# Kernel optimization log

Measured on AMD Instinct MI355X. Metric: run time of the kernel, lower is better.

Reference implementation:

```python
import jax, jax.numpy as jnp
import numpy as np

DIM_IN = 1024
DIM_K = 64
EPS = 1e-5

def setup_inputs() -> dict:
    key = jax.random.key(0)
    ks = jax.random.split(key, 9)
    s_in = 1.0 / np.sqrt(DIM_IN)
    s_k = 1.0 / np.sqrt(DIM_K)
    return {
        "X": jax.random.normal(ks[0], (8, 2048, DIM_IN), dtype=jnp.float32),
        "Wq": jax.random.uniform(ks[1], (DIM_IN, DIM_K), jnp.float32, -s_in, s_in),
        "bq": jax.random.uniform(ks[2], (DIM_K,), jnp.float32, -s_in, s_in),
        "Wk": jax.random.uniform(ks[3], (DIM_IN, DIM_K), jnp.float32, -s_in, s_in),
        "bk": jax.random.uniform(ks[4], (DIM_K,), jnp.float32, -s_in, s_in),
        "Wv": jax.random.uniform(ks[5], (DIM_IN, DIM_K), jnp.float32, -s_in, s_in),
        "bv": jax.random.uniform(ks[6], (DIM_K,), jnp.float32, -s_in, s_in),
        "Wo": jax.random.uniform(ks[7], (DIM_K, DIM_IN), jnp.float32, -s_k, s_k),
        "bo": jax.random.uniform(ks[8], (DIM_IN,), jnp.float32, -s_k, s_k),
        "gamma": jnp.ones((DIM_IN,), jnp.float32),
        "beta": jnp.zeros((DIM_IN,), jnp.float32),
    }

def reference(X, Wq, bq, Wk, bk, Wv, bv, Wo, bo, gamma, beta):
    q = X @ Wq + bq                       # [B,S,K]
    k = X @ Wk + bk
    v = X @ Wv + bv
    scores = jnp.einsum("bqk,bsk->bqs", q, k) / jnp.sqrt(jnp.float32(DIM_K))
    attn = jax.nn.softmax(scores, axis=2)  # [B,S,S]
    av = jnp.einsum("bqs,bsk->bqk", attn, v)
    y = X + av @ Wo + bo                  # residual, [B,S,D]
    mu = jnp.mean(y, axis=-1, keepdims=True)
    var = jnp.mean(jnp.square(y - mu), axis=-1, keepdims=True)
    return (y - mu) / jnp.sqrt(var + EPS) * gamma + beta
```

## Files before the change

### kernel.cpp

```cpp
#include <hip/hip_runtime.h>
#include <hip/hip_bf16.h>

#define DIM_D 1024
#define DIM_KH 64
#define SEQ   2048
#define BATCH 8
#define NROWS (BATCH*SEQ)
#define KVSPLIT 4
#define KEYS_PER_SPLIT (SEQ/KVSPLIT)

typedef __attribute__((ext_vector_type(8))) short short8;
typedef __attribute__((ext_vector_type(4))) short short4v;
typedef __attribute__((ext_vector_type(4))) float floatx4;

__device__ __forceinline__ ushort f2bf(float f) {
    union { __hip_bfloat16 h; ushort u; } cv;
    cv.h = __float2bfloat16(f);
    return cv.u;
}

__device__ __forceinline__ uint4 pack8(float4 a, float4 b) {
    uint4 p;
    p.x = (uint)f2bf(a.x) | ((uint)f2bf(a.y) << 16);
    p.y = (uint)f2bf(a.z) | ((uint)f2bf(a.w) << 16);
    p.z = (uint)f2bf(b.x) | ((uint)f2bf(b.y) << 16);
    p.w = (uint)f2bf(b.z) | ((uint)f2bf(b.w) << 16);
    return p;
}

__global__ void wcvt_kernel(const float* __restrict__ Wq,
                            const float* __restrict__ Wk,
                            const float* __restrict__ Wv,
                            ushort* __restrict__ WT)
{
    const int n  = blockIdx.x;
    const int o  = n >> 6;
    const int nn = n & 63;
    const float* W = (o == 0) ? Wq : (o == 1) ? Wk : Wv;
    #pragma unroll
    for (int i = 0; i < 4; i++) {
        int k = threadIdx.x + i * 256;
        WT[(size_t)n * DIM_D + k] = f2bf(W[(size_t)k * DIM_KH + nn]);
    }
}

__global__ void wocvt_kernel(const float* __restrict__ Wo, ushort* __restrict__ WoT)
{
    const int tid = threadIdx.x;
    const int n = blockIdx.x * 4 + (tid >> 6);
    const int k = tid & 63;
    WoT[(size_t)n * DIM_KH + k] = f2bf(Wo[(size_t)k * DIM_D + n]);
}

__global__ __launch_bounds__(256, 1) void qkv_mfma(
    const float* __restrict__ X, const ushort* __restrict__ WT,
    const float* __restrict__ bq, const float* __restrict__ bk,
    const float* __restrict__ bv,
    ushort* __restrict__ Qb, ushort* __restrict__ Kb, ushort* __restrict__ Vb)
{
    const int tid = threadIdx.x;
    const int m0  = blockIdx.x * 64;
    const int o   = blockIdx.y;

    __shared__ ushort Xs[2][64 * 64];
    __shared__ ushort Wls[2][64 * 64];

    const int w  = tid >> 6;
    const int l  = tid & 63;
    const int ql = l & 15;
    const int g  = (l >> 4) & 3;
    const int swz = (ql & 7) << 3;

    const int sr  = tid >> 2;
    const int sc  = (tid & 3) << 4;
    const int ssw = (sr & 7) << 3;
    const float*  Xrow = X  + (size_t)(m0 + sr) * DIM_D + sc;
    const ushort* Wrow = WT + (size_t)(o * 64 + sr) * DIM_D + sc;

    float4 xr[4];
    uint4  wr[2];

    floatx4 acc[4];
    #pragma unroll
    for (int fn = 0; fn < 4; fn++) acc[fn] = (floatx4){0.f, 0.f, 0.f, 0.f};

    #pragma unroll
    for (int f = 0; f < 4; f++)
        xr[f] = *reinterpret_cast<const float4*>(Xrow + f * 4);
    #pragma unroll
    for (int h = 0; h < 2; h++)
        wr[h] = *reinterpret_cast<const uint4*>(Wrow + h * 8);
    #pragma unroll
    for (int h = 0; h < 2; h++) {
        *reinterpret_cast<uint4*>(&Xs[0][sr * 64 + ((sc + h * 8) ^ ssw)]) =
            pack8(xr[2 * h], xr[2 * h + 1]);
        *reinterpret_cast<uint4*>(&Wls[0][sr * 64 + ((sc + h * 8) ^ ssw)]) = wr[h];
    }
    __syncthreads();

    #pragma unroll
    for (int t = 0; t < 16; t++) {
        const int cur = t & 1;
        const int nxt = cur ^ 1;
        if (t < 15) {
            const int k1 = (t + 1) * 64;
            #pragma unroll
            for (int f = 0; f < 4; f++)
                xr[f] = *reinterpret_cast<const float4*>(Xrow + k1 + f * 4);
            #pragma unroll
            for (int h = 0; h < 2; h++)
                wr[h] = *reinterpret_cast<const uint4*>(Wrow + k1 + h * 8);
        }

        #pragma unroll
        for (int kk = 0; kk < 2; kk++) {
            short8 a = *reinterpret_cast<const short8*>(
                &Xs[cur][(16 * w + ql) * 64 + ((kk * 32 + g * 8) ^ swz)]);
            #pragma unroll
            for (int fn = 0; fn < 4; fn++) {
                short8 b = *reinterpret_cast<const short8*>(
                    &Wls[cur][(16 * fn + ql) * 64 + ((kk * 32 + g * 8) ^ swz)]);
                acc[fn] = __builtin_amdgcn_mfma_f32_16x16x32_bf16(a, b, acc[fn], 0, 0, 0);
            }
        }

        if (t < 15) {
            #pragma unroll
            for (int h = 0; h < 2; h++) {
                *reinterpret_cast<uint4*>(&Xs[nxt][sr * 64 + ((sc + h * 8) ^ ssw)]) =
                    pack8(xr[2 * h], xr[2 * h + 1]);
                *reinterpret_cast<uint4*>(&Wls[nxt][sr * 64 + ((sc + h * 8) ^ ssw)]) = wr[h];
            }
        }
        __syncthreads();
    }

    const float* bias = (o == 0) ? bq : (o == 1) ? bk : bv;
    ushort* O = (o == 0) ? Qb : (o == 1) ? Kb : Vb;
    float bvreg[4];
    #pragma unroll
    for (int fn = 0; fn < 4; fn++) bvreg[fn] = bias[16 * fn + ql];

    #pragma unroll
    for (int fn = 0; fn < 4; fn++) {
        #pragma unroll
        for (int r = 0; r < 4; r++) {
            int row = m0 + 16 * w + 4 * g + r;
            O[(size_t)row * DIM_KH + 16 * fn + ql] = f2bf(acc[fn][r] + bvreg[fn]);
        }
    }
}

__global__ __launch_bounds__(256) void attn_mfma(
    const ushort* __restrict__ Qb, const ushort* __restrict__ Kb,
    const ushort* __restrict__ Vb,
    float* __restrict__ Opart, float* __restrict__ Ml)
{
    const int tid = threadIdx.x;
    const int w   = tid >> 6;
    const int l   = tid & 63;
    const int ql  = l & 15;
    const int g   = (l >> 4) & 3;
    const int q0  = blockIdx.x * 64;
    const int s   = blockIdx.y;
    const int b   = blockIdx.z;
    const int swzq = (ql & 7) << 3;

    __shared__ ushort Ks[64 * 64];
    __shared__ ushort VTs[64 * 64];

    short8 qf[2];
    #pragma unroll
    for (int kk = 0; kk < 2; kk++) {
        qf[kk] = *reinterpret_cast<const short8*>(
            Qb + ((size_t)(b * SEQ + q0 + 16 * w + ql)) * DIM_KH + kk * 32 + g * 8);
    }

    floatx4 accv[4];
    #pragma unroll
    for (int fd = 0; fd < 4; fd++) accv[fd] = (floatx4){0.f, 0.f, 0.f, 0.f};
    float m_run = -3.0e38f, l_run = 0.f;

    const ushort* Kbb = Kb + (size_t)b * SEQ * DIM_KH;
    const ushort* Vbb = Vb + (size_t)b * SEQ * DIM_KH;
    const int t_begin = s * KEYS_PER_SPLIT;
    const int t_end   = t_begin + KEYS_PER_SPLIT;

    for (int t0 = t_begin; t0 < t_end; t0 += 64) {
        __syncthreads();
        #pragma unroll
        for (int i = 0; i < 2; i++) {
            int idx = tid + i * 256;
            int row = idx >> 3;
            int ch  = idx & 7;
            uint4 v = *reinterpret_cast<const uint4*>(
                Kbb + (size_t)(t0 + row) * DIM_KH + ch * 8);
            *reinterpret_cast<uint4*>(&Ks[row * 64 + ((ch * 8) ^ ((row & 7) << 3))]) = v;
        }
        {
            int kg = tid >> 4, dg = tid & 15;
            int key0 = kg * 4, dim0 = dg * 4;
            uint2 vr[4];
            #pragma unroll
            for (int i = 0; i < 4; i++)
                vr[i] = *reinterpret_cast<const uint2*>(
                    Vbb + (size_t)(t0 + key0 + i) * DIM_KH + dim0);
            #pragma unroll
            for (int j = 0; j < 4; j++) {
                uint e0 = (j == 0) ? (vr[0].x & 0xffffu) : (j == 1) ? (vr[0].x >> 16)
                        : (j == 2) ? (vr[0].y & 0xffffu) : (vr[0].y >> 16);
                uint e1 = (j == 0) ? (vr[1].x & 0xffffu) : (j == 1) ? (vr[1].x >> 16)
                        : (j == 2) ? (vr[1].y & 0xffffu) : (vr[1].y >> 16);
                uint e2 = (j == 0) ? (vr[2].x & 0xffffu) : (j == 1) ? (vr[2].x >> 16)
                        : (j == 2) ? (vr[2].y & 0xffffu) : (vr[2].y >> 16);
                uint e3 = (j == 0) ? (vr[3].x & 0xffffu) : (j == 1) ? (vr[3].x >> 16)
                        : (j == 2) ? (vr[3].y & 0xffffu) : (vr[3].y >> 16);
                uint2 p; p.x = e0 | (e1 << 16); p.y = e2 | (e3 << 16);
                int dim = dim0 + j;
                int addr = dim * 64 + (key0 ^ ((dim & 15) << 2));
                *reinterpret_cast<uint2*>(&VTs[addr]) = p;
            }
        }
        __syncthreads();

        floatx4 sfrag[4];
        #pragma unroll
        for (int f = 0; f < 4; f++) {
            sfrag[f] = (floatx4){0.f, 0.f, 0.f, 0.f};
            #pragma unroll
            for (int kk = 0; kk < 2; kk++) {
                short8 a = *reinterpret_cast<const short8*>(
                    &Ks[(16 * f + ql) * 64 + ((kk * 32 + g * 8) ^ swzq)]);
                sfrag[f] = __builtin_amdgcn_mfma_f32_16x16x32_bf16(a, qf[kk], sfrag[f], 0, 0, 0);
            }
        }

        float mt = -3.0e38f;
        #pragma unroll
        for (int f = 0; f < 4; f++)
            #pragma unroll
            for (int r = 0; r < 4; r++) mt = fmaxf(mt, sfrag[f][r]);
        mt = fmaxf(mt, __shfl_xor(mt, 16));
        mt = fmaxf(mt, __shfl_xor(mt, 32));
        float m_new = fmaxf(m_run, mt);
        float sc = __expf((m_run - m_new) * 0.125f);
        float psum = 0.f;
        ushort pb[4][4];
        #pragma unroll
        for (int f = 0; f < 4; f++)
            #pragma unroll
            for (int r = 0; r < 4; r++) {
                float p = __expf((sfrag[f][r] - m_new) * 0.125f);
                pb[f][r] = f2bf(p);
                psum += p;
            }
        psum += __shfl_xor(psum, 16);
        psum += __shfl_xor(psum, 32);
        l_run = l_run * sc + psum;
        m_run = m_new;

        float s0 = __shfl(sc, 4 * g + 0);
        float s1 = __shfl(sc, 4 * g + 1);
        float s2 = __shfl(sc, 4 * g + 2);
        float s3 = __shfl(sc, 4 * g + 3);
        #pragma unroll
        for (int fd = 0; fd < 4; fd++) {
            accv[fd][0] *= s0; accv[fd][1] *= s1;
            accv[fd][2] *= s2; accv[fd][3] *= s3;
        }

        short8 pa_lo, pa_hi;
        pa_lo[0] = (short)pb[0][0]; pa_lo[1] = (short)pb[0][1];
        pa_lo[2] = (short)pb[0][2]; pa_lo[3] = (short)pb[0][3];
        pa_lo[4] = (short)pb[1][0]; pa_lo[5] = (short)pb[1][1];
        pa_lo[6] = (short)pb[1][2]; pa_lo[7] = (short)pb[1][3];
        pa_hi[0] = (short)pb[2][0]; pa_hi[1] = (short)pb[2][1];
        pa_hi[2] = (short)pb[2][2]; pa_hi[3] = (short)pb[2][3];
        pa_hi[4] = (short)pb[3][0]; pa_hi[5] = (short)pb[3][1];
        pa_hi[6] = (short)pb[3][2]; pa_hi[7] = (short)pb[3][3];

        #pragma unroll
        for (int fd = 0; fd < 4; fd++) {
            int dim = 16 * fd + ql;
            int base = dim * 64;
            int sw = (dim & 15) << 2;
            short4v v0 = *reinterpret_cast<const short4v*>(&VTs[base + ((4 * g) ^ sw)]);
            short4v v1 = *reinterpret_cast<const short4v*>(&VTs[base + ((16 + 4 * g) ^ sw)]);
            short8 bb;
            bb[0] = v0[0]; bb[1] = v0[1]; bb[2] = v0[2]; bb[3] = v0[3];
            bb[4] = v1[0]; bb[5] = v1[1]; bb[6] = v1[2]; bb[7] = v1[3];
            accv[fd] = __builtin_amdgcn_mfma_f32_16x16x32_bf16(pa_lo, bb, accv[fd], 0, 0, 0);
            short4v v2 = *reinterpret_cast<const short4v*>(&VTs[base + ((32 + 4 * g) ^ sw)]);
            short4v v3 = *reinterpret_cast<const short4v*>(&VTs[base + ((48 + 4 * g) ^ sw)]);
            short8 bb2;
            bb2[0] = v2[0]; bb2[1] = v2[1]; bb2[2] = v2[2]; bb2[3] = v2[3];
            bb2[4] = v3[0]; bb2[5] = v3[1]; bb2[6] = v3[2]; bb2[7] = v3[3];
            accv[fd] = __builtin_amdgcn_mfma_f32_16x16x32_bf16(pa_hi, bb2, accv[fd], 0, 0, 0);
        }
    }

    const size_t rid0 = (size_t)b * SEQ + q0;
    if (g == 0) {
        size_t rid = rid0 + 16 * w + ql;
        Ml[((size_t)s * NROWS + rid) * 2 + 0] = m_run;
        Ml[((size_t)s * NROWS + rid) * 2 + 1] = l_run;
    }
    #pragma unroll
    for (int fd = 0; fd < 4; fd++) {
        int col = 16 * fd + ql;
        size_t rbase = (size_t)s * NROWS + rid0 + 16 * w + 4 * g;
        Opart[(rbase + 0) * DIM_KH + col] = accv[fd][0];
        Opart[(rbase + 1) * DIM_KH + col] = accv[fd][1];
        Opart[(rbase + 2) * DIM_KH + col] = accv[fd][2];
        Opart[(rbase + 3) * DIM_KH + col] = accv[fd][3];
    }
}

__global__ __launch_bounds__(256) void attn_combine(
    const float* __restrict__ Opart, const float* __restrict__ Ml,
    ushort* __restrict__ AVb)
{
    const int tid = threadIdx.x;
    const size_t rid = (size_t)blockIdx.x * 16 + (tid >> 4);
    const int d0 = (tid & 15) * 4;

    float m[KVSPLIT], lv[KVSPLIT];
    float M = -3.0e38f;
    #pragma unroll
    for (int s = 0; s < KVSPLIT; s++) {
        m[s]  = Ml[((size_t)s * NROWS + rid) * 2 + 0];
        lv[s] = Ml[((size_t)s * NROWS + rid) * 2 + 1];
        M = fmaxf(M, m[s]);
    }
    float wsum = 0.f;
    float o0 = 0.f, o1 = 0.f, o2 = 0.f, o3 = 0.f;
    #pragma unroll
    for (int s = 0; s < KVSPLIT; s++) {
        float wgt = __expf((m[s] - M) * 0.125f);
        wsum = fmaf(wgt, lv[s], wsum);
        float4 a = *reinterpret_cast<const float4*>(
            Opart + ((size_t)s * NROWS + rid) * DIM_KH + d0);
        o0 = fmaf(wgt, a.x, o0);
        o1 = fmaf(wgt, a.y, o1);
        o2 = fmaf(wgt, a.z, o2);
        o3 = fmaf(wgt, a.w, o3);
    }
    float inv = 1.0f / wsum;
    uint2 p;
    p.x = (uint)f2bf(o0 * inv) | ((uint)f2bf(o1 * inv) << 16);
    p.y = (uint)f2bf(o2 * inv) | ((uint)f2bf(o3 * inv) << 16);
    *reinterpret_cast<uint2*>(AVb + rid * DIM_KH + d0) = p;
}

__global__ __launch_bounds__(256, 1) void out_mfma(
    const float* __restrict__ X, const ushort* __restrict__ AVb,
    const ushort* __restrict__ WoT, const float* __restrict__ bo,
    const float* __restrict__ gamma, const float* __restrict__ beta,
    float* __restrict__ Out)
{
    const int tid = threadIdx.x;
    const int w   = tid >> 6;
    const int l   = tid & 63;
    const int ql  = l & 15;
    const int g   = (l >> 4) & 3;
    const int row0 = blockIdx.x * 16;
    const int c0  = w * 256;

    __shared__ float Ls[16 * 1024];

    short8 bf0 = *reinterpret_cast<const short8*>(AVb + (size_t)(row0 + ql) * DIM_KH + g * 8);
    short8 bf1 = *reinterpret_cast<const short8*>(AVb + (size_t)(row0 + ql) * DIM_KH + 32 + g * 8);

    #pragma unroll
    for (int ft = 0; ft < 16; ft++) {
        const ushort* ap = WoT + (size_t)(c0 + 16 * ft + ql) * DIM_KH + g * 8;
        short8 a0 = *reinterpret_cast<const short8*>(ap);
        short8 a1 = *reinterpret_cast<const short8*>(ap + 32);
        floatx4 z = (floatx4){0.f, 0.f, 0.f, 0.f};
        z = __builtin_amdgcn_mfma_f32_16x16x32_bf16(a0, bf0, z, 0, 0, 0);
        z = __builtin_amdgcn_mfma_f32_16x16x32_bf16(a1, bf1, z, 0, 0, 0);
        int col = (c0 + 16 * ft + 4 * g) ^ ((ql & 7) << 2);
        *reinterpret_cast<floatx4*>(&Ls[ql * 1024 + col]) = z;
    }
    __syncthreads();

    const int r  = tid >> 4;
    const int cb = (tid & 15) * 4;
    const int rsw = (r & 7) << 2;
    const float* Xrow = X + (size_t)(row0 + r) * DIM_D;

    float4 yv[16];
    float s = 0.f, sq = 0.f;
    #pragma unroll
    for (int j = 0; j < 16; j++) {
        int col = cb + 64 * j;
        float4 a  = *reinterpret_cast<const float4*>(&Ls[r * 1024 + (col ^ rsw)]);
        float4 x4 = *reinterpret_cast<const float4*>(Xrow + col);
        float4 b4 = *reinterpret_cast<const float4*>(bo + col);
        float y0 = a.x + x4.x + b4.x;
        float y1 = a.y + x4.y + b4.y;
        float y2 = a.z + x4.z + b4.z;
        float y3 = a.w + x4.w + b4.w;
        yv[j] = (float4){y0, y1, y2, y3};
        s  += (y0 + y1) + (y2 + y3);
        sq += fmaf(y0, y0, fmaf(y1, y1, fmaf(y2, y2, y3 * y3)));
    }
    s  += __shfl_xor(s, 1);  s  += __shfl_xor(s, 2);
    s  += __shfl_xor(s, 4);  s  += __shfl_xor(s, 8);
    sq += __shfl_xor(sq, 1); sq += __shfl_xor(sq, 2);
    sq += __shfl_xor(sq, 4); sq += __shfl_xor(sq, 8);

    float mu  = s * (1.0f / 1024.0f);
    float var = fmaf(sq, (1.0f / 1024.0f), -mu * mu);
    float inv = rsqrtf(var + 1e-5f);

    float* Orow = Out + (size_t)(row0 + r) * DIM_D;
    #pragma unroll
    for (int j = 0; j < 16; j++) {
        int col = cb + 64 * j;
        float4 g4  = *reinterpret_cast<const float4*>(gamma + col);
        float4 be4 = *reinterpret_cast<const float4*>(beta + col);
        float4 ov;
        ov.x = fmaf((yv[j].x - mu) * inv, g4.x, be4.x);
        ov.y = fmaf((yv[j].y - mu) * inv, g4.y, be4.y);
        ov.z = fmaf((yv[j].z - mu) * inv, g4.z, be4.z);
        ov.w = fmaf((yv[j].w - mu) * inv, g4.w, be4.w);
        *reinterpret_cast<float4*>(Orow + col) = ov;
    }
}

extern "C" void kernel_launch(void* const* d_in, const int* in_sizes, int n_in,
                              void* d_out, int out_size, void* d_ws, size_t ws_size,
                              hipStream_t stream)
{
    (void)in_sizes; (void)n_in; (void)out_size; (void)ws_size;
    const float* X     = (const float*)d_in[0];
    const float* Wq    = (const float*)d_in[1];
    const float* bq    = (const float*)d_in[2];
    const float* Wk    = (const float*)d_in[3];
    const float* bk    = (const float*)d_in[4];
    const float* Wv    = (const float*)d_in[5];
    const float* bv    = (const float*)d_in[6];
    const float* Wo    = (const float*)d_in[7];
    const float* bo    = (const float*)d_in[8];
    const float* gamma = (const float*)d_in[9];
    const float* beta  = (const float*)d_in[10];
    float* Out = (float*)d_out;

    ushort* Qb  = (ushort*)d_ws;
    ushort* Kb  = Qb + (size_t)NROWS * DIM_KH;
    ushort* Vb  = Kb + (size_t)NROWS * DIM_KH;
    ushort* AVb = Vb + (size_t)NROWS * DIM_KH;
    ushort* WT  = AVb + (size_t)NROWS * DIM_KH;
    ushort* WoT = WT + (size_t)192 * DIM_D;
    float*  Opart = (float*)(WoT + (size_t)DIM_D * DIM_KH);
    float*  Ml    = Opart + (size_t)KVSPLIT * NROWS * DIM_KH;

    wcvt_kernel<<<192, 256, 0, stream>>>(Wq, Wk, Wv, WT);
    wocvt_kernel<<<256, 256, 0, stream>>>(Wo, WoT);
    qkv_mfma<<<dim3(256, 3), 256, 0, stream>>>(X, WT, bq, bk, bv, Qb, Kb, Vb);
    attn_mfma<<<dim3(SEQ/64, KVSPLIT, BATCH), 256, 0, stream>>>(Qb, Kb, Vb, Opart, Ml);
    attn_combine<<<NROWS/16, 256, 0, stream>>>(Opart, Ml, AVb);
    out_mfma<<<NROWS/16, 256, 0, stream>>>(X, AVb, WoT, bo, gamma, beta, Out);
}
```

Before: 98.18 us.

## Fuse split-KV combine into output projection, store partials as bf16, merge weight conversions

Removes the separate attn_combine kernel. Each out_mfma block now reads the per-split max/sum and partial outputs and forms the normalized AV fragments directly in registers before the Wo MFMA. Partial attention outputs are stored as bf16 instead of fp32, which halves that intermediate traffic but rounds the partials before the combine. The two weight-conversion kernels are merged into one launch, cutting launch count from six to four.

After: 95.17 us. 1.03x faster.

```diff
diff --git a/kernel.cpp b/kernel.cpp
--- a/kernel.cpp
+++ b/kernel.cpp
@@ -19,6 +19,12 @@
     return cv.u;
 }
 
+__device__ __forceinline__ float bf2f(ushort u) {
+    union { float f; uint u32; } c;
+    c.u32 = (uint)u << 16;
+    return c.f;
+}
+
 __device__ __forceinline__ uint4 pack8(float4 a, float4 b) {
     uint4 p;
     p.x = (uint)f2bf(a.x) | ((uint)f2bf(a.y) << 16);
@@ -28,28 +34,30 @@
     return p;
 }
 
-__global__ void wcvt_kernel(const float* __restrict__ Wq,
-                            const float* __restrict__ Wk,
-                            const float* __restrict__ Wv,
-                            ushort* __restrict__ WT)
-{
-    const int n  = blockIdx.x;
-    const int o  = n >> 6;
-    const int nn = n & 63;
-    const float* W = (o == 0) ? Wq : (o == 1) ? Wk : Wv;
-    #pragma unroll
-    for (int i = 0; i < 4; i++) {
-        int k = threadIdx.x + i * 256;
-        WT[(size_t)n * DIM_D + k] = f2bf(W[(size_t)k * DIM_KH + nn]);
-    }
-}
-
-__global__ void wocvt_kernel(const float* __restrict__ Wo, ushort* __restrict__ WoT)
+__global__ void wconv_all(const float* __restrict__ Wq,
+                          const float* __restrict__ Wk,
+                          const float* __restrict__ Wv,
+                          const float* __restrict__ Wo,
+                          ushort* __restrict__ WT,
+                          ushort* __restrict__ WoT)
 {
     const int tid = threadIdx.x;
-    const int n = blockIdx.x * 4 + (tid >> 6);
-    const int k = tid & 63;
-    WoT[(size_t)n * DIM_KH + k] = f2bf(Wo[(size_t)k * DIM_D + n]);
+    if (blockIdx.x < 192) {
+        const int n  = blockIdx.x;
+        const int o  = n >> 6;
+        const int nn = n & 63;
+        const float* W = (o == 0) ? Wq : (o == 1) ? Wk : Wv;
+        #pragma unroll
+        for (int i = 0; i < 4; i++) {
+            int k = tid + i * 256;
+            WT[(size_t)n * DIM_D + k] = f2bf(W[(size_t)k * DIM_KH + nn]);
+        }
+    } else {
+        const int blk = blockIdx.x - 192;
+        const int n = blk * 4 + (tid >> 6);
+        const int k = tid & 63;
+        WoT[(size_t)n * DIM_KH + k] = f2bf(Wo[(size_t)k * DIM_D + n]);
+    }
 }
 
 __global__ __launch_bounds__(256, 1) void qkv_mfma(
@@ -154,7 +162,7 @@
 __global__ __launch_bounds__(256) void attn_mfma(
     const ushort* __restrict__ Qb, const ushort* __restrict__ Kb,
     const ushort* __restrict__ Vb,
-    float* __restrict__ Opart, float* __restrict__ Ml)
+    ushort* __restrict__ OpartB, float* __restrict__ Ml)
 {
     const int tid = threadIdx.x;
     const int w   = tid >> 6;
@@ -309,51 +317,16 @@
     for (int fd = 0; fd < 4; fd++) {
         int col = 16 * fd + ql;
         size_t rbase = (size_t)s * NROWS + rid0 + 16 * w + 4 * g;
-        Opart[(rbase + 0) * DIM_KH + col] = accv[fd][0];
-        Opart[(rbase + 1) * DIM_KH + col] = accv[fd][1];
-        Opart[(rbase + 2) * DIM_KH + col] = accv[fd][2];
-        Opart[(rbase + 3) * DIM_KH + col] = accv[fd][3];
-    }
-}
-
-__global__ __launch_bounds__(256) void attn_combine(
-    const float* __restrict__ Opart, const float* __restrict__ Ml,
-    ushort* __restrict__ AVb)
-{
-    const int tid = threadIdx.x;
-    const size_t rid = (size_t)blockIdx.x * 16 + (tid >> 4);
-    const int d0 = (tid & 15) * 4;
-
-    float m[KVSPLIT], lv[KVSPLIT];
-    float M = -3.0e38f;
-    #pragma unroll
-    for (int s = 0; s < KVSPLIT; s++) {
-        m[s]  = Ml[((size_t)s * NROWS + rid) * 2 + 0];
-        lv[s] = Ml[((size_t)s * NROWS + rid) * 2 + 1];
-        M = fmaxf(M, m[s]);
-    }
-    float wsum = 0.f;
-    float o0 = 0.f, o1 = 0.f, o2 = 0.f, o3 = 0.f;
-    #pragma unroll
-    for (int s = 0; s < KVSPLIT; s++) {
-        float wgt = __expf((m[s] - M) * 0.125f);
-        wsum = fmaf(wgt, lv[s], wsum);
-        float4 a = *reinterpret_cast<const float4*>(
-            Opart + ((size_t)s * NROWS + rid) * DIM_KH + d0);
-        o0 = fmaf(wgt, a.x, o0);
-        o1 = fmaf(wgt, a.y, o1);
-        o2 = fmaf(wgt, a.z, o2);
-        o3 = fmaf(wgt, a.w, o3);
-    }
-    float inv = 1.0f / wsum;
-    uint2 p;
-    p.x = (uint)f2bf(o0 * inv) | ((uint)f2bf(o1 * inv) << 16);
-    p.y = (uint)f2bf(o2 * inv) | ((uint)f2bf(o3 * inv) << 16);
-    *reinterpret_cast<uint2*>(AVb + rid * DIM_KH + d0) = p;
+        OpartB[(rbase + 0) * DIM_KH + col] = f2bf(accv[fd][0]);
+        OpartB[(rbase + 1) * DIM_KH + col] = f2bf(accv[fd][1]);
+        OpartB[(rbase + 2) * DIM_KH + col] = f2bf(accv[fd][2]);
+        OpartB[(rbase + 3) * DIM_KH + col] = f2bf(accv[fd][3]);
+    }
 }
 
 __global__ __launch_bounds__(256, 1) void out_mfma(
-    const float* __restrict__ X, const ushort* __restrict__ AVb,
+    const float* __restrict__ X, const ushort* __restrict__ OpartB,
+    const float* __restrict__ Ml,
     const ushort* __restrict__ WoT, const float* __restrict__ bo,
     const float* __restrict__ gamma, const float* __restrict__ beta,
     float* __restrict__ Out)
@@ -368,8 +341,40 @@
 
     __shared__ float Ls[16 * 1024];
 
-    short8 bf0 = *reinterpret_cast<const short8*>(AVb + (size_t)(row0 + ql) * DIM_KH + g * 8);
-    short8 bf1 = *reinterpret_cast<const short8*>(AVb + (size_t)(row0 + ql) * DIM_KH + 32 + g * 8);
+    const size_t rid = (size_t)row0 + ql;
+    float m[KVSPLIT], lv[KVSPLIT];
+    float M = -3.0e38f;
+    #pragma unroll
+    for (int s = 0; s < KVSPLIT; s++) {
+        float2 t = *reinterpret_cast<const float2*>(Ml + ((size_t)s * NROWS + rid) * 2);
+        m[s] = t.x; lv[s] = t.y;
+        M = fmaxf(M, m[s]);
+    }
+    float wsum = 0.f;
+    float o[16];
+    #pragma unroll
+    for (int d = 0; d < 16; d++) o[d] = 0.f;
+    #pragma unroll
+    for (int s = 0; s < KVSPLIT; s++) {
+        float wgt = __expf((m[s] - M) * 0.125f);
+        wsum = fmaf(wgt, lv[s], wsum);
+        const ushort* op = OpartB + ((size_t)s * NROWS + rid) * DIM_KH;
+        union { uint4 u; ushort us[8]; } a, b;
+        a.u = *reinterpret_cast<const uint4*>(op + g * 8);
+        b.u = *reinterpret_cast<const uint4*>(op + 32 + g * 8);
+        #pragma unroll
+        for (int j = 0; j < 8; j++) {
+            o[j]     = fmaf(wgt, bf2f(a.us[j]), o[j]);
+            o[8 + j] = fmaf(wgt, bf2f(b.us[j]), o[8 + j]);
+        }
+    }
+    float avinv = 1.0f / wsum;
+    short8 bf0, bf1;
+    #pragma unroll
+    for (int j = 0; j < 8; j++) {
+        bf0[j] = (short)f2bf(o[j] * avinv);
+        bf1[j] = (short)f2bf(o[8 + j] * avinv);
+    }
 
     #pragma unroll
     for (int ft = 0; ft < 16; ft++) {
@@ -450,16 +455,13 @@
     ushort* Qb  = (ushort*)d_ws;
     ushort* Kb  = Qb + (size_t)NROWS * DIM_KH;
     ushort* Vb  = Kb + (size_t)NROWS * DIM_KH;
-    ushort* AVb = Vb + (size_t)NROWS * DIM_KH;
-    ushort* WT  = AVb + (size_t)NROWS * DIM_KH;
+    ushort* WT  = Vb + (size_t)NROWS * DIM_KH;
     ushort* WoT = WT + (size_t)192 * DIM_D;
-    float*  Opart = (float*)(WoT + (size_t)DIM_D * DIM_KH);
-    float*  Ml    = Opart + (size_t)KVSPLIT * NROWS * DIM_KH;
-
-    wcvt_kernel<<<192, 256, 0, stream>>>(Wq, Wk, Wv, WT);
-    wocvt_kernel<<<256, 256, 0, stream>>>(Wo, WoT);
+    ushort* OpartB = WoT + (size_t)DIM_D * DIM_KH;
+    float*  Ml  = (float*)(OpartB + (size_t)KVSPLIT * NROWS * DIM_KH);
+
+    wconv_all<<<448, 256, 0, stream>>>(Wq, Wk, Wv, Wo, WT, WoT);
     qkv_mfma<<<dim3(256, 3), 256, 0, stream>>>(X, WT, bq, bk, bv, Qb, Kb, Vb);
-    attn_mfma<<<dim3(SEQ/64, KVSPLIT, BATCH), 256, 0, stream>>>(Qb, Kb, Vb, Opart, Ml);
-    attn_combine<<<NROWS/16, 256, 0, stream>>>(Opart, Ml, AVb);
-    out_mfma<<<NROWS/16, 256, 0, stream>>>(X, AVb, WoT, bo, gamma, beta, Out);
-}
+    attn_mfma<<<dim3(SEQ/64, KVSPLIT, BATCH), 256, 0, stream>>>(Qb, Kb, Vb, OpartB, Ml);
+    out_mfma<<<NROWS/16, 256, 0, stream>>>(X, OpartB, Ml, WoT, bo, gamma, beta, Out);
+}
```
